# Optimization experiments

Hardware: AMD Instinct MI355X
Metric: run time of the kernel (lower is better)

## Reference

```python
import jax, jax.numpy as jnp
import numpy as np

D_MODEL = 1024
N_HEADS = 16
D_K = D_MODEL // N_HEADS


def setup_inputs() -> dict:
    key = jax.random.key(0)
    ks = jax.random.split(key, 12)
    B, S = 2, 2048
    scale = 1.0 / np.sqrt(D_MODEL)
    inp = {
        "q": jax.random.normal(ks[0], (B, S, D_MODEL), jnp.float32),
        "k": jax.random.normal(ks[1], (B, S, D_MODEL), jnp.float32),
        "v": jax.random.normal(ks[2], (B, S, D_MODEL), jnp.float32),
        "k_pe": jax.random.normal(ks[3], (N_HEADS, D_K, S), jnp.float32),
        "Wq": jax.random.normal(ks[4], (D_MODEL, D_MODEL), jnp.float32) * scale,
        "bq": jnp.zeros((D_MODEL,), jnp.float32),
        "Wk": jax.random.normal(ks[5], (D_MODEL, D_MODEL), jnp.float32) * scale,
        "bk": jnp.zeros((D_MODEL,), jnp.float32),
        "Wv": jax.random.normal(ks[6], (D_MODEL, D_MODEL), jnp.float32) * scale,
        "bv": jnp.zeros((D_MODEL,), jnp.float32),
        "Wo": jax.random.normal(ks[7], (D_MODEL, D_MODEL), jnp.float32) * scale,
        "bo": jnp.zeros((D_MODEL,), jnp.float32),
    }
    return inp


def reference(q, k, v, k_pe, Wq, bq, Wk, bk, Wv, bv, Wo, bo):
    B, S, _ = q.shape
    # projections -> [B, H, S, d_k]
    def split_heads(x):
        return x.reshape(B, S, N_HEADS, D_K).transpose(0, 2, 1, 3)
    qh = split_heads(q @ Wq + bq)
    kh = split_heads(k @ Wk + bk)
    vh = split_heads(v @ Wv + bv)
    # content scores + relative positional scores (two matmuls, summed)
    scores = jnp.einsum("bhsd,bhtd->bhst", qh, kh)
    scores = scores + jnp.einsum("bhsd,hdt->bhst", qh, k_pe)
    scores = scores / jnp.sqrt(jnp.asarray(D_K, qh.dtype))
    attn = jax.nn.softmax(scores, axis=-1)
    out = jnp.einsum("bhst,bhtd->bhsd", attn, vh)  # [B,H,S,d_k]
    out = out.transpose(0, 2, 1, 3).reshape(B, S, D_MODEL)
    return out @ Wo + bo
```

## Files before the change

kernel.cpp:

```cpp
#include <hip/hip_runtime.h>
#include <stdint.h>
#include <math.h>

typedef __bf16 bf16;
typedef __attribute__((ext_vector_type(8))) __bf16 bf16x8;
typedef __attribute__((ext_vector_type(4))) __bf16 bf16x4;
typedef __attribute__((ext_vector_type(4))) float f32x4;

#define MFMA_BF16(a, b, c) __builtin_amdgcn_mfma_f32_16x16x32_bf16((a), (b), (c), 0, 0, 0)

#if __has_builtin(__builtin_amdgcn_exp2f)
#define EXP2F __builtin_amdgcn_exp2f
#else
#define EXP2F exp2f
#endif

#define QSCALE 0.18033688011112042f

__device__ __forceinline__ void gl_lds16(const bf16* g, bf16* l) {
  __builtin_amdgcn_global_load_lds(
      (__attribute__((address_space(1))) unsigned int*)(uintptr_t)(g),
      (__attribute__((address_space(3))) unsigned int*)(l),
      16, 0, 0);
}

__global__ __launch_bounds__(256) void prep(
    const float* __restrict__ q, const float* __restrict__ k,
    const float* __restrict__ v, bf16* __restrict__ qb,
    bf16* __restrict__ kb, bf16* __restrict__ vb,
    const float* __restrict__ W0, const float* __restrict__ W1,
    const float* __restrict__ W2, const float* __restrict__ W3,
    bf16* __restrict__ Wt,
    const float* __restrict__ kpe, bf16* __restrict__ kpeb)
{
  __shared__ float tile[64][65];
  const int tid = threadIdx.x;
  const int bid = blockIdx.x;
  if (bid < 6144) {
    const int z = bid >> 11;
    const int idx = bid & 2047;
    const float* s = (z == 0) ? q : (z == 1) ? k : v;
    bf16* d = (z == 0) ? qb : (z == 1) ? kb : vb;
    size_t i = ((size_t)idx * 256 + tid) * 8;
    float4 a = *(const float4*)(s + i);
    float4 b = *(const float4*)(s + i + 4);
    bf16x8 o;
    o[0] = (bf16)a.x; o[1] = (bf16)a.y; o[2] = (bf16)a.z; o[3] = (bf16)a.w;
    o[4] = (bf16)b.x; o[5] = (bf16)b.y; o[6] = (bf16)b.z; o[7] = (bf16)b.w;
    *(bf16x8*)(d + i) = o;
  } else if (bid < 7168) {
    const int t = bid - 6144;
    const int z = t >> 8;
    const int rem = t & 255;
    const int r0 = (rem >> 4) * 64, c0 = (rem & 15) * 64;
    const float* src = (z == 0) ? W0 : (z == 1) ? W1 : (z == 2) ? W2 : W3;
    bf16* dst = Wt + (size_t)z * (1024 * 1024);
#pragma unroll
    for (int h = 0; h < 2; ++h) {
      int qq = tid + h * 256;
      int row = qq >> 3, cc = qq & 7;
      float4 a = *(const float4*)(src + (size_t)(r0 + row) * 1024 + c0 + cc * 8);
      float4 b = *(const float4*)(src + (size_t)(r0 + row) * 1024 + c0 + cc * 8 + 4);
      tile[row][cc * 8 + 0] = a.x; tile[row][cc * 8 + 1] = a.y;
      tile[row][cc * 8 + 2] = a.z; tile[row][cc * 8 + 3] = a.w;
      tile[row][cc * 8 + 4] = b.x; tile[row][cc * 8 + 5] = b.y;
      tile[row][cc * 8 + 6] = b.z; tile[row][cc * 8 + 7] = b.w;
    }
    __syncthreads();
#pragma unroll
    for (int h = 0; h < 2; ++h) {
      int qq = tid + h * 256;
      int row = qq >> 3, cc = qq & 7;
      bf16x8 o;
#pragma unroll
      for (int e = 0; e < 8; ++e) o[e] = (bf16)tile[cc * 8 + e][row];
      *(bf16x8*)(dst + (size_t)(c0 + row) * 1024 + r0 + cc * 8) = o;
    }
  } else {
    const int idx = bid - 7168;
    size_t i = ((size_t)idx * 256 + tid) * 8;
    float4 a = *(const float4*)(kpe + i);
    float4 b = *(const float4*)(kpe + i + 4);
    bf16x8 o;
    o[0] = (bf16)a.x; o[1] = (bf16)a.y; o[2] = (bf16)a.z; o[3] = (bf16)a.w;
    o[4] = (bf16)b.x; o[5] = (bf16)b.y; o[6] = (bf16)b.z; o[7] = (bf16)b.w;
    *(bf16x8*)(kpeb + i) = o;
  }
}

template <int MODE>
__device__ __forceinline__ void gemm_body256(
    const bf16* __restrict__ A, const bf16* __restrict__ Wt,
    const float* __restrict__ bias, float oscale,
    const bf16* __restrict__ kpeb, void* __restrict__ out_v,
    bf16* __restrict__ As, bf16* __restrict__ Bs)
{
  const int tid = threadIdx.x;
  const int w = tid >> 6, lane = tid & 63;
  const int lm = lane & 15, quad = lane >> 4;
  const int wm = w >> 2, wn = w & 3;
  const int lid = blockIdx.x + (blockIdx.y << 2);
  const int xcd = lid & 7, jj = lid >> 3;
  const int m0 = (xcd * 2 + (jj & 1)) * 256;
  const int n0 = (jj >> 1) * 256;

  f32x4 zero4 = {0.f, 0.f, 0.f, 0.f};
  f32x4 acc[4][4];
#pragma unroll
  for (int i = 0; i < 4; ++i)
#pragma unroll
    for (int j = 0; j < 4; ++j) acc[i][j] = zero4;

  auto stage = [&](int buf, int kb) {
    int row = tid >> 2, cs = tid & 3;
    int cc = cs ^ ((row >> 1) & 3);
    gl_lds16(A + (size_t)(m0 + row) * 1024 + kb * 32 + cc * 8,
             As + buf * 8192 + tid * 8);
    gl_lds16(Wt + (size_t)(n0 + row) * 1024 + kb * 32 + cc * 8,
             Bs + buf * 8192 + tid * 8);
  };

  stage(0, 0);
  stage(1, 1);

  int cur = 0;
  for (int kb = 0; kb < 32; ++kb) {
    if (kb < 30) {
      stage((kb + 2) % 3, kb + 2);
      asm volatile("s_waitcnt vmcnt(4)" ::: "memory");
    } else if (kb == 30) {
      asm volatile("s_waitcnt vmcnt(2)" ::: "memory");
    } else {
      asm volatile("s_waitcnt vmcnt(0)" ::: "memory");
    }
    __builtin_amdgcn_s_barrier();
    asm volatile("" ::: "memory");

    const bf16* Ab = As + cur * 8192;
    const bf16* Bb = Bs + cur * 8192;
    bf16x8 af[4], bfv[4];
#pragma unroll
    for (int i = 0; i < 4; ++i) {
      int row = wm * 64 + i * 16 + lm;
      af[i] = *(const bf16x8*)(Ab + row * 32 + ((quad ^ ((row >> 1) & 3)) * 8));
    }
#pragma unroll
    for (int j = 0; j < 4; ++j) {
      int row = wn * 64 + j * 16 + lm;
      bfv[j] = *(const bf16x8*)(Bb + row * 32 + ((quad ^ ((row >> 1) & 3)) * 8));
    }
#pragma unroll
    for (int i = 0; i < 4; ++i)
#pragma unroll
      for (int j = 0; j < 4; ++j)
        acc[i][j] = MFMA_BF16(af[i], bfv[j], acc[i][j]);

    __builtin_amdgcn_s_barrier();
    asm volatile("" ::: "memory");
    cur = (cur + 1) == 3 ? 0 : cur + 1;
  }

  const int ncol = n0 + wn * 64;
  float bv4[4];
#pragma unroll
  for (int j = 0; j < 4; ++j) bv4[j] = bias[ncol + j * 16 + lm];
#pragma unroll
  for (int i = 0; i < 4; ++i) {
    const int mbase = m0 + wm * 64 + i * 16 + quad * 4;
    const int b = mbase >> 11, s = mbase & 2047;
#pragma unroll
    for (int j = 0; j < 4; ++j) {
      const int ng = ncol + j * 16 + lm;
      const int hh = ng >> 6, d = ng & 63;
      if (MODE == 2) {
        bf16x4 o;
#pragma unroll
        for (int r = 0; r < 4; ++r) o[r] = (bf16)(acc[i][j][r] + bv4[j]);
        *(bf16x4*)((bf16*)out_v + ((size_t)(b * 16 + hh) * 64 + d) * 2048 + s) = o;
      } else if (MODE == 1) {
        bf16x4 p4 = *(const bf16x4*)(kpeb + ((size_t)(hh * 64 + d)) * 2048 + s);
#pragma unroll
        for (int r = 0; r < 4; ++r) {
          float val = acc[i][j][r] + bv4[j] + (float)p4[r];
          ((bf16*)out_v)[(((size_t)(b * 16 + hh)) * 2048 + (s + r)) * 64 + d] =
              (bf16)val;
        }
      } else {
#pragma unroll
        for (int r = 0; r < 4; ++r) {
          float val = acc[i][j][r] + bv4[j];
          ((bf16*)out_v)[(((size_t)(b * 16 + hh)) * 2048 + (s + r)) * 64 + d] =
              (bf16)(val * oscale);
        }
      }
    }
  }
}

__global__ __launch_bounds__(1024, 4) void qkv_gemm(
    const bf16* __restrict__ qb, const bf16* __restrict__ kb, const bf16* __restrict__ vb,
    const bf16* __restrict__ Wt, const float* __restrict__ biq,
    const float* __restrict__ bik, const float* __restrict__ biv,
    const bf16* __restrict__ kpeb,
    bf16* __restrict__ Qs, bf16* __restrict__ Ks, bf16* __restrict__ Vts)
{
  __shared__ __align__(16) bf16 As[3 * 256 * 32];
  __shared__ __align__(16) bf16 Bs[3 * 256 * 32];
  const int z = blockIdx.z;
  if (z == 0) {
    gemm_body256<0>(qb, Wt, biq, QSCALE, nullptr, Qs, As, Bs);
  } else if (z == 1) {
    gemm_body256<1>(kb, Wt + (size_t)1 * 1024 * 1024, bik, 1.f, kpeb, Ks, As, Bs);
  } else {
    gemm_body256<2>(vb, Wt + (size_t)2 * 1024 * 1024, biv, 1.f, nullptr, Vts, As, Bs);
  }
}

__global__ __launch_bounds__(256) void out_gemm(
    const bf16* __restrict__ A, const bf16* __restrict__ Wt,
    const float* __restrict__ bias, float* __restrict__ out)
{
  __shared__ __align__(16) bf16 As[3 * 128 * 32];
  __shared__ __align__(16) bf16 Bs[3 * 128 * 32];
  const int tid = threadIdx.x;
  const int w = tid >> 6, lane = tid & 63;
  const int lm = lane & 15, quad = lane >> 4;
  const int wr = w >> 1, wc = w & 1;
  const int lid = blockIdx.x + (blockIdx.y << 3);
  const int xcd = lid & 7, j = lid >> 3;
  const int m0 = (xcd * 4 + (j & 3)) * 128;
  const int n0 = (j >> 2) * 128;

  f32x4 zero4 = {0.f, 0.f, 0.f, 0.f};
  f32x4 acc[4][4];
#pragma unroll
  for (int i = 0; i < 4; ++i)
#pragma unroll
    for (int jj = 0; jj < 4; ++jj) acc[i][jj] = zero4;

  auto stage = [&](int buf, int kb) {
#pragma unroll
    for (int h = 0; h < 2; ++h) {
      int qq = tid + h * 256;
      int row = qq >> 2, cs = qq & 3;
      int cc = cs ^ ((row >> 1) & 3);
      gl_lds16(A + (size_t)(m0 + row) * 1024 + kb * 32 + cc * 8,
               As + buf * 4096 + qq * 8);
      gl_lds16(Wt + (size_t)(n0 + row) * 1024 + kb * 32 + cc * 8,
               Bs + buf * 4096 + qq * 8);
    }
  };

  stage(0, 0);
  stage(1, 1);

  int cur = 0;
  for (int kb = 0; kb < 32; ++kb) {
    if (kb < 30) {
      stage((kb + 2) % 3, kb + 2);
      asm volatile("s_waitcnt vmcnt(8)" ::: "memory");
    } else if (kb == 30) {
      asm volatile("s_waitcnt vmcnt(4)" ::: "memory");
    } else {
      asm volatile("s_waitcnt vmcnt(0)" ::: "memory");
    }
    __builtin_amdgcn_s_barrier();
    asm volatile("" ::: "memory");

    const bf16* Ab = As + cur * 4096;
    const bf16* Bb = Bs + cur * 4096;
    bf16x8 af[4], bfv[4];
#pragma unroll
    for (int i = 0; i < 4; ++i) {
      int row = wr * 64 + i * 16 + lm;
      af[i] = *(const bf16x8*)(Ab + row * 32 + ((quad ^ ((row >> 1) & 3)) * 8));
    }
#pragma unroll
    for (int jj = 0; jj < 4; ++jj) {
      int row = wc * 64 + jj * 16 + lm;
      bfv[jj] = *(const bf16x8*)(Bb + row * 32 + ((quad ^ ((row >> 1) & 3)) * 8));
    }
#pragma unroll
    for (int i = 0; i < 4; ++i)
#pragma unroll
      for (int jj = 0; jj < 4; ++jj)
        acc[i][jj] = MFMA_BF16(af[i], bfv[jj], acc[i][jj]);

    __builtin_amdgcn_s_barrier();
    asm volatile("" ::: "memory");
    cur = (cur + 1) == 3 ? 0 : cur + 1;
  }

  const int ncol = n0 + wc * 64;
  float bv4[4];
#pragma unroll
  for (int jj = 0; jj < 4; ++jj) bv4[jj] = bias[ncol + jj * 16 + lm];
#pragma unroll
  for (int i = 0; i < 4; ++i) {
    const int mbase = m0 + wr * 64 + i * 16 + quad * 4;
#pragma unroll
    for (int jj = 0; jj < 4; ++jj) {
      const int ng = ncol + jj * 16 + lm;
#pragma unroll
      for (int r = 0; r < 4; ++r) {
        out[(size_t)(mbase + r) * 1024 + ng] = acc[i][jj][r] + bv4[jj];
      }
    }
  }
}

__global__ __launch_bounds__(512) void flash_attn(
    const bf16* __restrict__ Q, const bf16* __restrict__ K,
    const bf16* __restrict__ Vt, bf16* __restrict__ O)
{
  __shared__ __align__(16) bf16 QtPs[128 * 72];
  __shared__ __align__(16) bf16 Kt[2][64 * 64];
  __shared__ __align__(16) bf16 Vs[2][64 * 64];
  bf16* Ps = QtPs;

  const int tid = threadIdx.x;
  const int w = tid >> 6, lane = tid & 63;
  const int lm = lane & 15, quad = lane >> 4;
  const int id = blockIdx.x;
  const int xcd = id & 7, j = id >> 3;
  const int bh = xcd * 4 + (j & 3);
  const int s0 = (j >> 2) * 128;
  const size_t qkbase = (size_t)bh * (2048 * 64);
  const size_t vbase = (size_t)bh * (64 * 2048);

#pragma unroll
  for (int h = 0; h < 2; ++h) {
    int qq = tid + h * 512;
    int row = qq >> 3, cs = qq & 7;
    int cc = cs ^ (row & 7);
    gl_lds16(Q + qkbase + (size_t)(s0 + row) * 64 + cc * 8, QtPs + qq * 8);
  }
  {
    int row = tid >> 3, cs = tid & 7;
    int cc = cs ^ (row & 7);
    gl_lds16(K + qkbase + (size_t)row * 64 + cc * 8, Kt[0] + tid * 8);
    gl_lds16(Vt + vbase + (size_t)row * 2048 + cc * 8, Vs[0] + tid * 8);
  }
  __syncthreads();

  bf16x8 qa0, qa1;
  {
    int row = w * 16 + lm;
    qa0 = *(const bf16x8*)(QtPs + row * 64 + ((quad ^ (row & 7)) * 8));
    qa1 = *(const bf16x8*)(QtPs + row * 64 + (((quad + 4) ^ (row & 7)) * 8));
  }
  __syncthreads();

  f32x4 zero4 = {0.f, 0.f, 0.f, 0.f};
  float l_part = 0.f;
  f32x4 oacc[4];
#pragma unroll
  for (int dt = 0; dt < 4; ++dt) oacc[dt] = zero4;

  const int prow = (w * 16 + lm) * 72;

  for (int kt = 0; kt < 32; ++kt) {
    const int cur = kt & 1;
    if (kt < 31) {
      const int t1 = (kt + 1) * 64;
      int row = tid >> 3, cs = tid & 7;
      int cc = cs ^ (row & 7);
      gl_lds16(K + qkbase + (size_t)(t1 + row) * 64 + cc * 8, Kt[cur ^ 1] + tid * 8);
      gl_lds16(Vt + vbase + (size_t)row * 2048 + t1 + cc * 8, Vs[cur ^ 1] + tid * 8);
    }

#pragma unroll
    for (int c = 0; c < 4; ++c) {
      int row = c * 16 + lm;
      bf16x8 kb0 = *(const bf16x8*)(Kt[cur] + row * 64 + ((quad ^ (row & 7)) * 8));
      bf16x8 kb1 = *(const bf16x8*)(Kt[cur] + row * 64 + (((quad + 4) ^ (row & 7)) * 8));
      __builtin_amdgcn_s_setprio(1);
      f32x4 z = MFMA_BF16(kb0, qa0, zero4);
      f32x4 st = MFMA_BF16(kb1, qa1, z);
      __builtin_amdgcn_s_setprio(0);
      bf16x4 pk;
#pragma unroll
      for (int r = 0; r < 4; ++r) {
        float p = EXP2F(st[r]);
        l_part += p;
        pk[r] = (bf16)p;
      }
      *(bf16x4*)(Ps + prow + c * 16 + quad * 4) = pk;
    }

    bf16x8 pa0 = *(const bf16x8*)(Ps + prow + quad * 8);
    bf16x8 pa1 = *(const bf16x8*)(Ps + prow + 32 + quad * 8);
#pragma unroll
    for (int dt = 0; dt < 4; ++dt) {
      int row = dt * 16 + lm;
      bf16x8 va0 = *(const bf16x8*)(Vs[cur] + row * 64 + ((quad ^ (row & 7)) * 8));
      bf16x8 va1 = *(const bf16x8*)(Vs[cur] + row * 64 + (((quad + 4) ^ (row & 7)) * 8));
      __builtin_amdgcn_s_setprio(1);
      oacc[dt] = MFMA_BF16(va0, pa0, oacc[dt]);
      oacc[dt] = MFMA_BF16(va1, pa1, oacc[dt]);
      __builtin_amdgcn_s_setprio(0);
    }

    __syncthreads();
  }

  float l = l_part;
  l += __shfl_xor(l, 16, 64);
  l += __shfl_xor(l, 32, 64);
  float inv = 1.f / l;
#pragma unroll
  for (int dt = 0; dt < 4; ++dt)
#pragma unroll
    for (int r = 0; r < 4; ++r)
      Ps[prow + dt * 16 + quad * 4 + r] = (bf16)(oacc[dt][r] * inv);

  const int b = bh >> 4, hh = bh & 15;
  const int srow = s0 + w * 16 + lm;
  const size_t ob = ((size_t)(b * 2048 + srow)) * 1024 + hh * 64;
#pragma unroll
  for (int half = 0; half < 2; ++half) {
    bf16x8 ov = *(const bf16x8*)(Ps + prow + (half * 4 + quad) * 8);
    *(bf16x8*)(O + ob + (half * 4 + quad) * 8) = ov;
  }
}

extern "C" void kernel_launch(void* const* d_in, const int* in_sizes, int n_in,
                              void* d_out, int out_size, void* d_ws, size_t ws_size,
                              hipStream_t stream) {
  (void)in_sizes; (void)n_in; (void)out_size; (void)ws_size;
  const float* q   = (const float*)d_in[0];
  const float* k   = (const float*)d_in[1];
  const float* v   = (const float*)d_in[2];
  const float* kpe = (const float*)d_in[3];
  const float* Wq  = (const float*)d_in[4];
  const float* bq  = (const float*)d_in[5];
  const float* Wk  = (const float*)d_in[6];
  const float* bk  = (const float*)d_in[7];
  const float* Wv  = (const float*)d_in[8];
  const float* bv  = (const float*)d_in[9];
  const float* Wo  = (const float*)d_in[10];
  const float* bo  = (const float*)d_in[11];

  const size_t NT = 4u * 1024 * 1024;
  bf16* ws  = (bf16*)d_ws;
  bf16* Wt  = ws;
  bf16* qb  = Wt + NT;
  bf16* kb  = qb + NT;
  bf16* vb  = kb + NT;
  bf16* Qs  = vb + NT;
  bf16* Ks  = Qs + NT;
  bf16* Vts = Ks + NT;
  bf16* Oa  = Vts + NT;
  bf16* kpeb = Oa;

  prep<<<dim3(8192), 256, 0, stream>>>(q, k, v, qb, kb, vb, Wq, Wk, Wv, Wo, Wt,
                                       kpe, kpeb);
  qkv_gemm<<<dim3(4, 16, 3), 1024, 0, stream>>>(qb, kb, vb, Wt, bq, bk, bv, kpeb,
                                                Qs, Ks, Vts);
  flash_attn<<<dim3(512), 512, 0, stream>>>(Qs, Ks, Vts, Oa);
  out_gemm<<<dim3(8, 32), 256, 0, stream>>>(Oa, Wt + 3u * 1024 * 1024, bo,
                                            (float*)d_out);
}
```

Before: 233.6 us.

## Split attention KV range across two blocks and merge with combine kernel

Flash attention now splits the 32 key tiles into two halves handled by separate blocks, doubling the grid from 512 to 1024. Each block writes unnormalized partial outputs (fp32 or bf16) plus row sums, and a new combine kernel adds the halves, normalizes, and writes bf16 for the output GEMM. The workspace layout is reshuffled (Wo moved to slot 0, lbuf placed where Wq used to be) to make room for the partials. The aim is more parallelism and better CU occupancy, at the cost of extra global traffic and one more launch. The split relies on no running max being used, since the scores are assumed bounded.

New measurement: 243.3 us. 4.2% more time.

```diff
diff --git a/kernel.cpp b/kernel.cpp
--- a/kernel.cpp
+++ b/kernel.cpp
@@ -23,6 +23,7 @@
       (__attribute__((address_space(3))) unsigned int*)(l),
       16, 0, 0);
 }
+
 
 __global__ __launch_bounds__(256) void prep(
     const float* __restrict__ q, const float* __restrict__ k,
@@ -54,7 +55,7 @@
     const int rem = t & 255;
     const int r0 = (rem >> 4) * 64, c0 = (rem & 15) * 64;
     const float* src = (z == 0) ? W0 : (z == 1) ? W1 : (z == 2) ? W2 : W3;
-    bf16* dst = Wt + (size_t)z * (1024 * 1024);
+    bf16* dst = Wt + (size_t)((z + 1) & 3) * (1024 * 1024);
 #pragma unroll
     for (int h = 0; h < 2; ++h) {
       int qq = tid + h * 256;
@@ -206,13 +207,14 @@
 {
   __shared__ __align__(16) bf16 As[3 * 256 * 32];
   __shared__ __align__(16) bf16 Bs[3 * 256 * 32];
+  const size_t M1 = 1024 * 1024;
   const int z = blockIdx.z;
   if (z == 0) {
-    gemm_body256<0>(qb, Wt, biq, QSCALE, nullptr, Qs, As, Bs);
+    gemm_body256<0>(qb, Wt + 1 * M1, biq, QSCALE, nullptr, Qs, As, Bs);
   } else if (z == 1) {
-    gemm_body256<1>(kb, Wt + (size_t)1 * 1024 * 1024, bik, 1.f, kpeb, Ks, As, Bs);
+    gemm_body256<1>(kb, Wt + 2 * M1, bik, 1.f, kpeb, Ks, As, Bs);
   } else {
-    gemm_body256<2>(vb, Wt + (size_t)2 * 1024 * 1024, biv, 1.f, nullptr, Vts, As, Bs);
+    gemm_body256<2>(vb, Wt + 3 * M1, biv, 1.f, nullptr, Vts, As, Bs);
   }
 }
 
@@ -311,7 +313,8 @@
 
 __global__ __launch_bounds__(512) void flash_attn(
     const bf16* __restrict__ Q, const bf16* __restrict__ K,
-    const bf16* __restrict__ Vt, bf16* __restrict__ O)
+    const bf16* __restrict__ Vt, float* __restrict__ Op1,
+    void* __restrict__ Op2, int op2f32, float* __restrict__ lbuf)
 {
   __shared__ __align__(16) bf16 QtPs[128 * 72];
   __shared__ __align__(16) bf16 Kt[2][64 * 64];
@@ -324,7 +327,10 @@
   const int id = blockIdx.x;
   const int xcd = id & 7, j = id >> 3;
   const int bh = xcd * 4 + (j & 3);
-  const int s0 = (j >> 2) * 128;
+  const int jj = j >> 2;
+  const int s0 = (jj & 15) * 128;
+  const int half = jj >> 4;
+  const int kt0 = half * 16;
   const size_t qkbase = (size_t)bh * (2048 * 64);
   const size_t vbase = (size_t)bh * (64 * 2048);
 
@@ -338,8 +344,8 @@
   {
     int row = tid >> 3, cs = tid & 7;
     int cc = cs ^ (row & 7);
-    gl_lds16(K + qkbase + (size_t)row * 64 + cc * 8, Kt[0] + tid * 8);
-    gl_lds16(Vt + vbase + (size_t)row * 2048 + cc * 8, Vs[0] + tid * 8);
+    gl_lds16(K + qkbase + (size_t)(kt0 * 64 + row) * 64 + cc * 8, Kt[0] + tid * 8);
+    gl_lds16(Vt + vbase + (size_t)row * 2048 + kt0 * 64 + cc * 8, Vs[0] + tid * 8);
   }
   __syncthreads();
 
@@ -359,10 +365,10 @@
 
   const int prow = (w * 16 + lm) * 72;
 
-  for (int kt = 0; kt < 32; ++kt) {
-    const int cur = kt & 1;
-    if (kt < 31) {
-      const int t1 = (kt + 1) * 64;
+  for (int it = 0; it < 16; ++it) {
+    const int cur = it & 1;
+    if (it < 15) {
+      const int t1 = (kt0 + it + 1) * 64;
       int row = tid >> 3, cs = tid & 7;
       int cc = cs ^ (row & 7);
       gl_lds16(K + qkbase + (size_t)(t1 + row) * 64 + cc * 8, Kt[cur ^ 1] + tid * 8);
@@ -407,27 +413,76 @@
   float l = l_part;
   l += __shfl_xor(l, 16, 64);
   l += __shfl_xor(l, 32, 64);
-  float inv = 1.f / l;
-#pragma unroll
-  for (int dt = 0; dt < 4; ++dt)
-#pragma unroll
-    for (int r = 0; r < 4; ++r)
-      Ps[prow + dt * 16 + quad * 4 + r] = (bf16)(oacc[dt][r] * inv);
+  if (quad == 0) lbuf[half * 65536 + bh * 2048 + s0 + w * 16 + lm] = l;
 
   const int b = bh >> 4, hh = bh & 15;
-  const int srow = s0 + w * 16 + lm;
-  const size_t ob = ((size_t)(b * 2048 + srow)) * 1024 + hh * 64;
-#pragma unroll
-  for (int half = 0; half < 2; ++half) {
-    bf16x8 ov = *(const bf16x8*)(Ps + prow + (half * 4 + quad) * 8);
-    *(bf16x8*)(O + ob + (half * 4 + quad) * 8) = ov;
-  }
+  float* Psf = (float*)QtPs;
+#pragma unroll
+  for (int p = 0; p < 2; ++p) {
+    __syncthreads();
+    if ((w >> 2) == p) {
+      int sl = (w & 3) * 16 + lm;
+#pragma unroll
+      for (int dt = 0; dt < 4; ++dt)
+#pragma unroll
+        for (int r = 0; r < 4; ++r)
+          Psf[sl * 68 + dt * 16 + quad * 4 + r] = oacc[dt][r];
+    }
+    __syncthreads();
+#pragma unroll
+    for (int e = 0; e < 2; ++e) {
+      int c = tid * 2 + e;
+      int rrow = c >> 4, c4 = c & 15;
+      float4 v4 = *(const float4*)(Psf + rrow * 68 + c4 * 4);
+      size_t gofs = ((size_t)(b * 2048 + s0 + p * 64 + rrow)) * 1024 + hh * 64 + c4 * 4;
+      if (half == 0) {
+        *(float4*)(Op1 + gofs) = v4;
+      } else if (op2f32) {
+        *(float4*)((float*)Op2 + gofs) = v4;
+      } else {
+        bf16x4 o;
+        o[0] = (bf16)v4.x; o[1] = (bf16)v4.y; o[2] = (bf16)v4.z; o[3] = (bf16)v4.w;
+        *(bf16x4*)((bf16*)Op2 + gofs) = o;
+      }
+    }
+  }
+}
+
+__global__ __launch_bounds__(256) void combine(
+    const float* __restrict__ Op1, const void* __restrict__ Op2, int op2f32,
+    const float* __restrict__ lbuf, bf16* __restrict__ Oa)
+{
+  size_t idx = ((size_t)blockIdx.x * 256 + threadIdx.x) * 8;
+  int row = (int)(idx >> 10);
+  int col = (int)(idx & 1023);
+  int hh = col >> 6;
+  int bh = ((row >> 11) << 4) + hh;
+  int srow = row & 2047;
+  float inv = 1.f / (lbuf[bh * 2048 + srow] + lbuf[65536 + bh * 2048 + srow]);
+  float4 a0 = *(const float4*)(Op1 + idx);
+  float4 a1 = *(const float4*)(Op1 + idx + 4);
+  float o[8] = {a0.x, a0.y, a0.z, a0.w, a1.x, a1.y, a1.z, a1.w};
+  if (op2f32) {
+    const float* p2 = (const float*)Op2;
+    float4 b0 = *(const float4*)(p2 + idx);
+    float4 b1 = *(const float4*)(p2 + idx + 4);
+    o[0] += b0.x; o[1] += b0.y; o[2] += b0.z; o[3] += b0.w;
+    o[4] += b1.x; o[5] += b1.y; o[6] += b1.z; o[7] += b1.w;
+  } else {
+    bf16x8 b8 = *(const bf16x8*)((const bf16*)Op2 + idx);
+#pragma unroll
+    for (int jj = 0; jj < 8; ++jj) o[jj] += (float)b8[jj];
+  }
+  bf16x8 r;
+#pragma unroll
+  for (int jj = 0; jj < 8; ++jj) r[jj] = (bf16)(o[jj] * inv);
+  *(bf16x8*)(Oa + idx) = r;
 }
 
 extern "C" void kernel_launch(void* const* d_in, const int* in_sizes, int n_in,
                               void* d_out, int out_size, void* d_ws, size_t ws_size,
                               hipStream_t stream) {
-  (void)in_sizes; (void)n_in; (void)out_size; (void)ws_size;
+  (void)in_sizes; (void)n_in; (void)out_size;
   const float* q   = (const float*)d_in[0];
   const float* k   = (const float*)d_in[1];
   const float* v   = (const float*)d_in[2];
@@ -441,23 +496,29 @@
   const float* Wo  = (const float*)d_in[10];
   const float* bo  = (const float*)d_in[11];
 
-  const size_t NT = 4u * 1024 * 1024;
-  bf16* ws  = (bf16*)d_ws;
-  bf16* Wt  = ws;
-  bf16* qb  = Wt + NT;
-  bf16* kb  = qb + NT;
-  bf16* vb  = kb + NT;
-  bf16* Qs  = vb + NT;
-  bf16* Ks  = Qs + NT;
-  bf16* Vts = Ks + NT;
-  bf16* Oa  = Vts + NT;
-  bf16* kpeb = Oa;
+  const size_t M1 = 1024 * 1024;
+  bf16* ws   = (bf16*)d_ws;
+  bf16* Wt   = ws;
+  bf16* Qs   = ws + 4 * M1;
+  bf16* Ks   = ws + 8 * M1;
+  bf16* Vts  = ws + 12 * M1;
+  bf16* Oa   = ws + 16 * M1;
+  bf16* kpeb = ws + 16 * M1;
+  bf16* qb   = ws + 20 * M1;
+  bf16* kb   = ws + 24 * M1;
+  bf16* vb   = ws + 28 * M1;
+  float* Op1 = (float*)(ws + 20 * M1);
+  float* lbuf = (float*)(ws + 1 * M1);
+  int op2f32 = ws_size >= (size_t)80 * 1024 * 1024 ? 1 : 0;
+  void* Op2  = op2f32 ? (void*)(ws + 32 * M1)
+                      : (void*)(ws + 28 * M1);
 
   prep<<<dim3(8192), 256, 0, stream>>>(q, k, v, qb, kb, vb, Wq, Wk, Wv, Wo, Wt,
                                        kpe, kpeb);
-  qkv_gemm<<<dim3(4, 16, 3), 1024, 0, stream>>>(qb, kb, vb, Wt, bq, bk, bv, kpeb,
-                                                Qs, Ks, Vts);
-  flash_attn<<<dim3(512), 512, 0, stream>>>(Qs, Ks, Vts, Oa);
-  out_gemm<<<dim3(8, 32), 256, 0, stream>>>(Oa, Wt + 3u * 1024 * 1024, bo,
-                                            (float*)d_out);
-}
+  qkv_gemm<<<dim3(4, 16, 3), 1024, 0, stream>>>(qb, kb, vb, Wt, bq, bk, bv,
+                                                kpeb, Qs, Ks, Vts);
+  flash_attn<<<dim3(1024), 512, 0, stream>>>(Qs, Ks, Vts, Op1, Op2, op2f32,
+                                             lbuf);
+  combine<<<dim3(2048), 256, 0, stream>>>(Op1, Op2, op2f32, lbuf, Oa);
+  out_gemm<<<dim3(8, 32), 256, 0, stream>>>(Oa, Wt, bo, (float*)d_out);
+}
```
